# Kernel tuning notes

Measured on AMD Instinct MI355X. Metric: run time of the kernel, lower is better.

Reference implementation:

```python
import jax, jax.numpy as jnp
import numpy as np

B, H, S, D = 2, 16, 2048, 64
NEG_INF = -1e30


def setup_inputs() -> dict:
    key = jax.random.key(0)
    kq, kk, kv = jax.random.split(key, 3)
    one = jnp.ones((1,), dtype=jnp.float32)
    return {
        "q": jax.random.normal(kq, (B, H, S, D), dtype=jnp.float32),
        "k": jax.random.normal(kk, (B, H, S, D), dtype=jnp.float32),
        "v": jax.random.normal(kv, (B, H, S, D), dtype=jnp.float32),
        "d_scale_q": one,
        "d_scale_k": one,
        "d_scale_v": one,
        "q_scale_s": one,
        "q_scale_o": one,
        "d_scale_s": one,
    }


def reference(q, k, v, d_scale_q, d_scale_k, d_scale_v, q_scale_s, q_scale_o, d_scale_s):
    # fp8 fused SDPA math (scales modeled exactly; fp8 rounding omitted in reference)
    scale = 1.0 / jnp.sqrt(jnp.asarray(D, q.dtype))
    qf = q * d_scale_q  # dequantized Q
    kf = k * d_scale_k  # dequantized K
    vf = v * d_scale_v  # dequantized V
    s = jnp.einsum("bhqd,bhkd->bhqk", qf, kf) * scale  # [B,H,S,S]
    # causal mask
    causal = jnp.tril(jnp.ones((S, S), dtype=bool))
    s = jnp.where(causal[None, None], s, NEG_INF)
    p = jax.nn.softmax(s, axis=-1)  # softmax probs
    amax_s = jnp.max(jnp.abs(p))  # amax of softmax output before requant
    # requantize probs (q_scale_s) then dequantize (d_scale_s) for PV matmul
    p_dq = p * (q_scale_s * d_scale_s)
    o_raw = jnp.einsum("bhqk,bhkd->bhqd", p_dq, vf)
    amax_o = jnp.max(jnp.abs(o_raw))  # amax of output before quantization
    o = o_raw * q_scale_o  # quantized-scale output
    return (o, amax_s, amax_o)
```

## Files before the change

### kernel.cpp

```cpp
#include <hip/hip_runtime.h>

#define BB 2
#define HH 16
#define SS 2048
#define DD 64

constexpr int OSIZE = BB * HH * SS * DD;
constexpr float LOG2E = 1.4426950408889634f;

using bf16x8 = __attribute__((ext_vector_type(8))) short;
using f32x4  = __attribute__((ext_vector_type(4))) float;
using u16x8  = __attribute__((ext_vector_type(8))) unsigned short;
using u32x2  = __attribute__((ext_vector_type(2))) unsigned int;
using fl4    = __attribute__((ext_vector_type(4))) float;

__device__ __forceinline__ unsigned short f2bf(float f) {
    unsigned int u = __float_as_uint(f);
    return (unsigned short)((u + 0x7fffu + ((u >> 16) & 1u)) >> 16);
}

__device__ __forceinline__ unsigned int pkbf(float lo, float hi) {
    return __builtin_amdgcn_perm(__float_as_uint(hi), __float_as_uint(lo), 0x07060302u);
}

__device__ __forceinline__ void atomicMaxPosF(float* addr, float v) {
    atomicMax(reinterpret_cast<unsigned int*>(addr), __float_as_uint(v));
}

__global__ __launch_bounds__(256) void prep_kv_kernel(
    const float* __restrict__ k, const float* __restrict__ v,
    const float* __restrict__ dsk, const float* __restrict__ dsv,
    unsigned short* __restrict__ kbf, unsigned short* __restrict__ vtb,
    float* __restrict__ out)
{
    const int t  = threadIdx.x;
    const int s0 = blockIdx.x * 64;
    const int bh = blockIdx.y;
    if (blockIdx.x == 0 && bh == 0 && t < 2) out[OSIZE + t] = 0.0f;

    const size_t base = (size_t)bh * SS * DD;
    const float sck = dsk[0], scv = dsv[0];

    {
        const float* kp = k + base + (size_t)s0 * DD + t * 16;
        unsigned short* ko = kbf + base + (size_t)s0 * DD + t * 16;
        fl4 a0 = ((const fl4*)kp)[0], a1 = ((const fl4*)kp)[1];
        fl4 a2 = ((const fl4*)kp)[2], a3 = ((const fl4*)kp)[3];
        u16x8 o0, o1;
        #pragma unroll
        for (int j = 0; j < 4; ++j) {
            o0[j] = f2bf(a0[j] * sck); o0[j + 4] = f2bf(a1[j] * sck);
            o1[j] = f2bf(a2[j] * sck); o1[j + 4] = f2bf(a3[j] * sck);
        }
        ((u16x8*)ko)[0] = o0; ((u16x8*)ko)[1] = o1;
    }

    __shared__ unsigned short T[64 * 72];
    {
        const int r  = t >> 2;
        const int cb = (t & 3) * 16;
        const fl4* vp = (const fl4*)(v + base + (size_t)(s0 + r) * DD + cb);
        unsigned short tmp[16];
        #pragma unroll
        for (int c = 0; c < 4; ++c) {
            fl4 x = vp[c];
            #pragma unroll
            for (int j = 0; j < 4; ++j) tmp[c * 4 + j] = f2bf(x[j] * scv);
        }
        *(u16x8*)&T[r * 72 + cb]     = *(u16x8*)&tmp[0];
        *(u16x8*)&T[r * 72 + cb + 8] = *(u16x8*)&tmp[8];
    }
    __syncthreads();
    {
        const int dr = t >> 2;
        const int sb = (t & 3) * 16;
        unsigned short tmp[16];
        #pragma unroll
        for (int j = 0; j < 16; ++j) tmp[j] = T[(sb + j) * 72 + dr];
        unsigned short* op = vtb + base + (size_t)dr * SS + s0 + sb;
        *(u16x8*)op       = *(u16x8*)&tmp[0];
        *(u16x8*)(op + 8) = *(u16x8*)&tmp[8];
    }
}

__global__ __launch_bounds__(256, 4) void fattn_kernel(
    const float* __restrict__ q,
    const unsigned short* __restrict__ kbf,
    const unsigned short* __restrict__ vtb,
    const float* __restrict__ dsq, const float* __restrict__ qss,
    const float* __restrict__ qso, const float* __restrict__ dss,
    float* __restrict__ out)
{
    const int x  = blockIdx.x;
    const int bh = blockIdx.y;
    const int tid  = threadIdx.x;
    const int wave = tid >> 6;
    const int lane = tid & 63;
    const int m16  = lane & 15;
    const int quad = lane >> 4;
    const int m7   = m16 & 7;

    __shared__ __align__(16) unsigned short Ksh[2][64 * 64];
    __shared__ __align__(16) unsigned short Vsh[2][64 * 64];
    __shared__ __align__(16) unsigned short Psh[4][16 * 64];

    const float q_scale = dsq[0] * 0.125f * LOG2E;
    const size_t base = (size_t)bh * SS * DD;
    const unsigned short* kbh = kbf + base;
    const unsigned short* vbh = vtb + base;

    const int kr0  = tid >> 3;
    const int kcs  = ((tid & 7) ^ (kr0 & 7)) * 8;
    const int koff0 = kr0 * DD + kcs, koff1 = koff0 + 32 * DD;
    const int voff0 = kr0 * SS + kcs, voff1 = voff0 + 32 * SS;
    const int lds0 = tid * 8, lds1 = (tid + 256) * 8;

    const int gsw0 = (quad ^ m7) * 8;
    const int gsw1 = ((4 | quad) ^ m7) * 8;

    const float ss_ = qss[0] * dss[0];
    const float o_q = qso[0];
    float amax_o = 0.0f, amax_s = 0.0f;

    #pragma unroll
    for (int pass = 0; pass < 2; ++pass) {
        const int qt = pass ? (31 - x) : x;
        const int qb = qt * 64;
        const int nkt = qt + 1;

        bf16x8 qf[2];
        {
            const int qrow = qb + wave * 16 + m16;
            const float* qp = q + base + (size_t)qrow * DD + quad * 8;
            #pragma unroll
            for (int f = 0; f < 2; ++f) {
                fl4 a = *(const fl4*)(qp + f * 32);
                fl4 b = *(const fl4*)(qp + f * 32 + 4);
                #pragma unroll
                for (int j = 0; j < 4; ++j) {
                    qf[f][j]     = (short)f2bf(a[j] * q_scale);
                    qf[f][j + 4] = (short)f2bf(b[j] * q_scale);
                }
            }
        }

        f32x4 Oacc[4];
        #pragma unroll
        for (int dt = 0; dt < 4; ++dt)
            #pragma unroll
            for (int r = 0; r < 4; ++r) Oacc[dt][r] = 0.0f;

        float l_lane = 0.0f, e_max = 0.0f;

        {
            u16x8 k0 = *(const u16x8*)(kbh + koff0);
            u16x8 k1 = *(const u16x8*)(kbh + koff1);
            u16x8 v0 = *(const u16x8*)(vbh + voff0);
            u16x8 v1 = *(const u16x8*)(vbh + voff1);
            *(u16x8*)&Ksh[0][lds0] = k0; *(u16x8*)&Ksh[0][lds1] = k1;
            *(u16x8*)&Vsh[0][lds0] = v0; *(u16x8*)&Vsh[0][lds1] = v1;
        }
        __syncthreads();

        for (int t = 0; t < nkt; ++t) {
            const int b = t & 1;
            const bool pf = (t + 1 < nkt);

            u16x8 kp0, kp1, vp0, vp1;
            if (pf) {
                const unsigned short* kg = kbh + (size_t)(t + 1) * 64 * DD;
                const unsigned short* vg = vbh + (t + 1) * 64;
                kp0 = *(const u16x8*)(kg + koff0);
                kp1 = *(const u16x8*)(kg + koff1);
                vp0 = *(const u16x8*)(vg + voff0);
                vp1 = *(const u16x8*)(vg + voff1);
            }

            const unsigned short* Kt = &Ksh[b][0];
            const unsigned short* Vt = &Vsh[b][0];

            f32x4 sacc[4];
            #pragma unroll
            for (int nt = 0; nt < 4; ++nt) {
                f32x4 acc = {0.0f, 0.0f, 0.0f, 0.0f};
                const int rb = (nt * 16 + m16) * 64;
                bf16x8 kf0 = *(const bf16x8*)&Kt[rb + gsw0];
                bf16x8 kf1 = *(const bf16x8*)&Kt[rb + gsw1];
                acc = __builtin_amdgcn_mfma_f32_16x16x32_bf16(kf0, qf[0], acc, 0, 0, 0);
                acc = __builtin_amdgcn_mfma_f32_16x16x32_bf16(kf1, qf[1], acc, 0, 0, 0);
                sacc[nt] = acc;
            }

            if (t == nkt - 1) {
                const int qg = qb + wave * 16 + m16;
                const int kb = t * 64;
                #pragma unroll
                for (int nt = 0; nt < 4; ++nt)
                    #pragma unroll
                    for (int r = 0; r < 4; ++r) {
                        const int kc = kb + nt * 16 + quad * 4 + r;
                        if (kc > qg) sacc[nt][r] = -1.0e30f;
                    }
            }

            #pragma unroll
            for (int nt = 0; nt < 4; ++nt)
                #pragma unroll
                for (int r = 0; r < 4; ++r) {
                    const float e = __builtin_amdgcn_exp2f(sacc[nt][r]);
                    sacc[nt][r] = e;
                    e_max  = fmaxf(e_max, e);
                    l_lane += e;
                }

            unsigned short* P = &Psh[wave][0];
            #pragma unroll
            for (int nt = 0; nt < 4; ++nt) {
                u32x2 pk;
                pk[0] = pkbf(sacc[nt][0], sacc[nt][1]);
                pk[1] = pkbf(sacc[nt][2], sacc[nt][3]);
                const int g = nt * 2 + (quad >> 1);
                *(u32x2*)&P[m16 * 64 + ((g ^ m7) * 8) + (quad & 1) * 4] = pk;
            }
            bf16x8 pf0 = *(const bf16x8*)&P[m16 * 64 + gsw0];
            bf16x8 pf1 = *(const bf16x8*)&P[m16 * 64 + gsw1];

            #pragma unroll
            for (int dt = 0; dt < 4; ++dt) {
                const int rb = (dt * 16 + m16) * 64;
                bf16x8 vf0 = *(const bf16x8*)&Vt[rb + gsw0];
                bf16x8 vf1 = *(const bf16x8*)&Vt[rb + gsw1];
                Oacc[dt] = __builtin_amdgcn_mfma_f32_16x16x32_bf16(pf0, vf0, Oacc[dt], 0, 0, 0);
                Oacc[dt] = __builtin_amdgcn_mfma_f32_16x16x32_bf16(pf1, vf1, Oacc[dt], 0, 0, 0);
            }

            if (pf) {
                *(u16x8*)&Ksh[b ^ 1][lds0] = kp0; *(u16x8*)&Ksh[b ^ 1][lds1] = kp1;
                *(u16x8*)&Vsh[b ^ 1][lds0] = vp0; *(u16x8*)&Vsh[b ^ 1][lds1] = vp1;
            }
            __syncthreads();
        }

        float l = l_lane;
        l += __shfl_xor(l, 16);
        l += __shfl_xor(l, 32);
        float em = e_max;
        em = fmaxf(em, __shfl_xor(em, 16));
        em = fmaxf(em, __shfl_xor(em, 32));
        amax_s = fmaxf(amax_s, em / l);

        #pragma unroll
        for (int r = 0; r < 4; ++r) {
            const float lr  = __shfl(l, (lane & 48) | (quad * 4 + r));
            const float ivl = ss_ / lr;
            const int row = qb + wave * 16 + quad * 4 + r;
            float* op = out + base + (size_t)row * DD + m16;
            #pragma unroll
            for (int dt = 0; dt < 4; ++dt) {
                const float o_raw = Oacc[dt][r] * ivl;
                amax_o = fmaxf(amax_o, fabsf(o_raw));
                op[dt * 16] = o_raw * o_q;
            }
        }
    }

    #pragma unroll
    for (int m = 1; m < 64; m <<= 1) {
        amax_o = fmaxf(amax_o, __shfl_xor(amax_o, m));
        amax_s = fmaxf(amax_s, __shfl_xor(amax_s, m));
    }
    if (lane == 0) {
        atomicMaxPosF(out + OSIZE,     amax_s);
        atomicMaxPosF(out + OSIZE + 1, amax_o);
    }
}

extern "C" void kernel_launch(void* const* d_in, const int* in_sizes, int n_in,
                              void* d_out, int out_size, void* d_ws, size_t ws_size,
                              hipStream_t stream) {
    const float* q   = (const float*)d_in[0];
    const float* k   = (const float*)d_in[1];
    const float* v   = (const float*)d_in[2];
    const float* dsq = (const float*)d_in[3];
    const float* dsk = (const float*)d_in[4];
    const float* dsv = (const float*)d_in[5];
    const float* qss = (const float*)d_in[6];
    const float* qso = (const float*)d_in[7];
    const float* dss = (const float*)d_in[8];
    float* out = (float*)d_out;

    unsigned short* kbf = (unsigned short*)d_ws;
    unsigned short* vtb = (unsigned short*)d_ws + OSIZE;

    prep_kv_kernel<<<dim3(SS / 64, BB * HH), 256, 0, stream>>>(k, v, dsk, dsv, kbf, vtb, out);

    dim3 grid(16, BB * HH);
    fattn_kernel<<<grid, 256, 0, stream>>>(q, kbf, vtb, dsq, qss, qso, dss, out);
}
```

Measured before the change: 184.5 us.

## Split KV tiles across two wave groups per block and combine partials in LDS

Blocks grow to 512 threads, split into two groups of four waves. Each group processes alternating KV tiles for the same query tile with its own double-buffered K/V LDS, then group 1 hands its O accumulator and row sums to group 0 through LDS for the final normalisation. This is meant to halve each block's serial KV loop and raise the number of waves per CU. The cost is double the LDS per block, an extra combine step with barriers, and odd tile counts that leave one group idle on the last iteration. The grid is also reordered so that bh is the fast-varying block index.

```diff
diff --git a/kernel.cpp b/kernel.cpp
--- a/kernel.cpp
+++ b/kernel.cpp
@@ -83,7 +83,7 @@
     }
 }
 
-__global__ __launch_bounds__(256, 4) void fattn_kernel(
+__global__ __launch_bounds__(512, 4) void fattn_kernel(
     const float* __restrict__ q,
     const unsigned short* __restrict__ kbf,
     const unsigned short* __restrict__ vtb,
@@ -91,29 +91,32 @@
     const float* __restrict__ qso, const float* __restrict__ dss,
     float* __restrict__ out)
 {
-    const int x  = blockIdx.x;
-    const int bh = blockIdx.y;
-    const int tid  = threadIdx.x;
-    const int wave = tid >> 6;
-    const int lane = tid & 63;
-    const int m16  = lane & 15;
-    const int quad = lane >> 4;
-    const int m7   = m16 & 7;
-
-    __shared__ __align__(16) unsigned short Ksh[2][64 * 64];
-    __shared__ __align__(16) unsigned short Vsh[2][64 * 64];
-    __shared__ __align__(16) unsigned short Psh[4][16 * 64];
+    const int bh = blockIdx.x;
+    const int x  = blockIdx.y;
+    const int tid   = threadIdx.x;
+    const int group = tid >> 8;
+    const int tg    = tid & 255;
+    const int wave  = tid >> 6;
+    const int gw    = wave & 3;
+    const int lane  = tid & 63;
+    const int m16   = lane & 15;
+    const int quad  = lane >> 4;
+    const int m7    = m16 & 7;
+
+    __shared__ __align__(16) unsigned short Ksh[2][2][64 * 64];
+    __shared__ __align__(16) unsigned short Vsh[2][2][64 * 64];
+    __shared__ __align__(16) unsigned short Psh[8][16 * 64];
 
     const float q_scale = dsq[0] * 0.125f * LOG2E;
     const size_t base = (size_t)bh * SS * DD;
     const unsigned short* kbh = kbf + base;
     const unsigned short* vbh = vtb + base;
 
-    const int kr0  = tid >> 3;
-    const int kcs  = ((tid & 7) ^ (kr0 & 7)) * 8;
+    const int kr0  = tg >> 3;
+    const int kcs  = ((tg & 7) ^ (kr0 & 7)) * 8;
     const int koff0 = kr0 * DD + kcs, koff1 = koff0 + 32 * DD;
     const int voff0 = kr0 * SS + kcs, voff1 = voff0 + 32 * SS;
-    const int lds0 = tid * 8, lds1 = (tid + 256) * 8;
+    const int lds0 = tg * 8, lds1 = (tg + 256) * 8;
 
     const int gsw0 = (quad ^ m7) * 8;
     const int gsw1 = ((4 | quad) ^ m7) * 8;
@@ -122,15 +125,18 @@
     const float o_q = qso[0];
     float amax_o = 0.0f, amax_s = 0.0f;
 
-    #pragma unroll
+    float* CombO = (float*)&Ksh[1][0][0];
+    float* CombL = (float*)&Vsh[1][0][0];
+
     for (int pass = 0; pass < 2; ++pass) {
         const int qt = pass ? (31 - x) : x;
         const int qb = qt * 64;
         const int nkt = qt + 1;
+        const int n_iter = (nkt + 1) >> 1;
 
         bf16x8 qf[2];
         {
-            const int qrow = qb + wave * 16 + m16;
+            const int qrow = qb + gw * 16 + m16;
             const float* qp = q + base + (size_t)qrow * DD + quad * 8;
             #pragma unroll
             for (int f = 0; f < 2; ++f) {
@@ -149,129 +155,157 @@
         for (int dt = 0; dt < 4; ++dt)
             #pragma unroll
             for (int r = 0; r < 4; ++r) Oacc[dt][r] = 0.0f;
-
         float l_lane = 0.0f, e_max = 0.0f;
 
-        {
-            u16x8 k0 = *(const u16x8*)(kbh + koff0);
-            u16x8 k1 = *(const u16x8*)(kbh + koff1);
-            u16x8 v0 = *(const u16x8*)(vbh + voff0);
-            u16x8 v1 = *(const u16x8*)(vbh + voff1);
-            *(u16x8*)&Ksh[0][lds0] = k0; *(u16x8*)&Ksh[0][lds1] = k1;
-            *(u16x8*)&Vsh[0][lds0] = v0; *(u16x8*)&Vsh[0][lds1] = v1;
+        if (group < nkt) {
+            const unsigned short* kg = kbh + (size_t)group * 64 * DD;
+            const unsigned short* vg = vbh + group * 64;
+            u16x8 k0 = *(const u16x8*)(kg + koff0);
+            u16x8 k1 = *(const u16x8*)(kg + koff1);
+            u16x8 v0 = *(const u16x8*)(vg + voff0);
+            u16x8 v1 = *(const u16x8*)(vg + voff1);
+            *(u16x8*)&Ksh[group][0][lds0] = k0; *(u16x8*)&Ksh[group][0][lds1] = k1;
+            *(u16x8*)&Vsh[group][0][lds0] = v0; *(u16x8*)&Vsh[group][0][lds1] = v1;
         }
         __syncthreads();
 
-        for (int t = 0; t < nkt; ++t) {
-            const int b = t & 1;
-            const bool pf = (t + 1 < nkt);
+        for (int j = 0; j < n_iter; ++j) {
+            const int b  = j & 1;
+            const int tt = 2 * j + group;
+            const int tn = tt + 2;
+            const bool pfv = (tn < nkt);
 
             u16x8 kp0, kp1, vp0, vp1;
-            if (pf) {
-                const unsigned short* kg = kbh + (size_t)(t + 1) * 64 * DD;
-                const unsigned short* vg = vbh + (t + 1) * 64;
+            if (pfv) {
+                const unsigned short* kg = kbh + (size_t)tn * 64 * DD;
+                const unsigned short* vg = vbh + tn * 64;
                 kp0 = *(const u16x8*)(kg + koff0);
                 kp1 = *(const u16x8*)(kg + koff1);
                 vp0 = *(const u16x8*)(vg + voff0);
                 vp1 = *(const u16x8*)(vg + voff1);
             }
 
-            const unsigned short* Kt = &Ksh[b][0];
-            const unsigned short* Vt = &Vsh[b][0];
-
-            f32x4 sacc[4];
-            #pragma unroll
-            for (int nt = 0; nt < 4; ++nt) {
-                f32x4 acc = {0.0f, 0.0f, 0.0f, 0.0f};
-                const int rb = (nt * 16 + m16) * 64;
-                bf16x8 kf0 = *(const bf16x8*)&Kt[rb + gsw0];
-                bf16x8 kf1 = *(const bf16x8*)&Kt[rb + gsw1];
-                acc = __builtin_amdgcn_mfma_f32_16x16x32_bf16(kf0, qf[0], acc, 0, 0, 0);
-                acc = __builtin_amdgcn_mfma_f32_16x16x32_bf16(kf1, qf[1], acc, 0, 0, 0);
-                sacc[nt] = acc;
-            }
-
-            if (t == nkt - 1) {
-                const int qg = qb + wave * 16 + m16;
-                const int kb = t * 64;
+            if (tt < nkt) {
+                const unsigned short* Kt = &Ksh[group][b][0];
+                const unsigned short* Vt = &Vsh[group][b][0];
+
+                f32x4 sacc[4];
+                #pragma unroll
+                for (int nt = 0; nt < 4; ++nt) {
+                    f32x4 acc = {0.0f, 0.0f, 0.0f, 0.0f};
+                    const int rb = (nt * 16 + m16) * 64;
+                    bf16x8 kf0 = *(const bf16x8*)&Kt[rb + gsw0];
+                    bf16x8 kf1 = *(const bf16x8*)&Kt[rb + gsw1];
+                    acc = __builtin_amdgcn_mfma_f32_16x16x32_bf16(kf0, qf[0], acc, 0, 0, 0);
+                    acc = __builtin_amdgcn_mfma_f32_16x16x32_bf16(kf1, qf[1], acc, 0, 0, 0);
+                    sacc[nt] = acc;
+                }
+
+                if (tt == nkt - 1) {
+                    const int qg = qb + gw * 16 + m16;
+                    const int kb = tt * 64;
+                    #pragma unroll
+                    for (int nt = 0; nt < 4; ++nt)
+                        #pragma unroll
+                        for (int r = 0; r < 4; ++r) {
+                            const int kc = kb + nt * 16 + quad * 4 + r;
+                            if (kc > qg) sacc[nt][r] = -1.0e30f;
+                        }
+                }
+
                 #pragma unroll
                 for (int nt = 0; nt < 4; ++nt)
                     #pragma unroll
                     for (int r = 0; r < 4; ++r) {
-                        const int kc = kb + nt * 16 + quad * 4 + r;
-                        if (kc > qg) sacc[nt][r] = -1.0e30f;
+                        const float e = __builtin_amdgcn_exp2f(sacc[nt][r]);
+                        sacc[nt][r] = e;
+                        e_max  = fmaxf(e_max, e);
+                        l_lane += e;
                     }
-            }
-
-            #pragma unroll
-            for (int nt = 0; nt < 4; ++nt)
-                #pragma unroll
-                for (int r = 0; r < 4; ++r) {
-                    const float e = __builtin_amdgcn_exp2f(sacc[nt][r]);
-                    sacc[nt][r] = e;
-                    e_max  = fmaxf(e_max, e);
-                    l_lane += e;
-                }
-
-            unsigned short* P = &Psh[wave][0];
-            #pragma unroll
-            for (int nt = 0; nt < 4; ++nt) {
-                u32x2 pk;
-                pk[0] = pkbf(sacc[nt][0], sacc[nt][1]);
-                pk[1] = pkbf(sacc[nt][2], sacc[nt][3]);
-                const int g = nt * 2 + (quad >> 1);
-                *(u32x2*)&P[m16 * 64 + ((g ^ m7) * 8) + (quad & 1) * 4] = pk;
-            }
-            bf16x8 pf0 = *(const bf16x8*)&P[m16 * 64 + gsw0];
-            bf16x8 pf1 = *(const bf16x8*)&P[m16 * 64 + gsw1];
-
+
+                unsigned short* P = &Psh[wave][0];
+                #pragma unroll
+                for (int nt = 0; nt < 4; ++nt) {
+                    u32x2 pk;
+                    pk[0] = pkbf(sacc[nt][0], sacc[nt][1]);
+                    pk[1] = pkbf(sacc[nt][2], sacc[nt][3]);
+                    const int g = nt * 2 + (quad >> 1);
+                    *(u32x2*)&P[m16 * 64 + ((g ^ m7) * 8) + (quad & 1) * 4] = pk;
+                }
+                bf16x8 pf0 = *(const bf16x8*)&P[m16 * 64 + gsw0];
+                bf16x8 pf1 = *(const bf16x8*)&P[m16 * 64 + gsw1];
+
+                #pragma unroll
+                for (int dt = 0; dt < 4; ++dt) {
+                    const int rb = (dt * 16 + m16) * 64;
+                    bf16x8 vf0 = *(const bf16x8*)&Vt[rb + gsw0];
+                    bf16x8 vf1 = *(const bf16x8*)&Vt[rb + gsw1];
+                    Oacc[dt] = __builtin_amdgcn_mfma_f32_16x16x32_bf16(pf0, vf0, Oacc[dt], 0, 0, 0);
+                    Oacc[dt] = __builtin_amdgcn_mfma_f32_16x16x32_bf16(pf1, vf1, Oacc[dt], 0, 0, 0);
+                }
+            }
+
+            if (pfv) {
+                *(u16x8*)&Ksh[group][b ^ 1][lds0] = kp0; *(u16x8*)&Ksh[group][b ^ 1][lds1] = kp1;
+                *(u16x8*)&Vsh[group][b ^ 1][lds0] = vp0; *(u16x8*)&Vsh[group][b ^ 1][lds1] = vp1;
+            }
+            __syncthreads();
+        }
+
+        if (group == 1) {
+            float* co = CombO + gw * 1024;
+            #pragma unroll
+            for (int dt = 0; dt < 4; ++dt) *(f32x4*)(co + dt * 256 + lane * 4) = Oacc[dt];
+            CombL[gw * 64 + lane]       = l_lane;
+            CombL[256 + gw * 64 + lane] = e_max;
+        }
+        __syncthreads();
+        if (group == 0) {
+            const float* co = CombO + gw * 1024;
             #pragma unroll
             for (int dt = 0; dt < 4; ++dt) {
-                const int rb = (dt * 16 + m16) * 64;
-                bf16x8 vf0 = *(const bf16x8*)&Vt[rb + gsw0];
-                bf16x8 vf1 = *(const bf16x8*)&Vt[rb + gsw1];
-                Oacc[dt] = __builtin_amdgcn_mfma_f32_16x16x32_bf16(pf0, vf0, Oacc[dt], 0, 0, 0);
-                Oacc[dt] = __builtin_amdgcn_mfma_f32_16x16x32_bf16(pf1, vf1, Oacc[dt], 0, 0, 0);
-            }
-
-            if (pf) {
-                *(u16x8*)&Ksh[b ^ 1][lds0] = kp0; *(u16x8*)&Ksh[b ^ 1][lds1] = kp1;
-                *(u16x8*)&Vsh[b ^ 1][lds0] = vp0; *(u16x8*)&Vsh[b ^ 1][lds1] = vp1;
-            }
-            __syncthreads();
-        }
-
-        float l = l_lane;
-        l += __shfl_xor(l, 16);
-        l += __shfl_xor(l, 32);
-        float em = e_max;
-        em = fmaxf(em, __shfl_xor(em, 16));
-        em = fmaxf(em, __shfl_xor(em, 32));
-        amax_s = fmaxf(amax_s, em / l);
-
-        #pragma unroll
-        for (int r = 0; r < 4; ++r) {
-            const float lr  = __shfl(l, (lane & 48) | (quad * 4 + r));
-            const float ivl = ss_ / lr;
-            const int row = qb + wave * 16 + quad * 4 + r;
-            float* op = out + base + (size_t)row * DD + m16;
-            #pragma unroll
-            for (int dt = 0; dt < 4; ++dt) {
-                const float o_raw = Oacc[dt][r] * ivl;
-                amax_o = fmaxf(amax_o, fabsf(o_raw));
-                op[dt * 16] = o_raw * o_q;
-            }
-        }
-    }
-
-    #pragma unroll
-    for (int m = 1; m < 64; m <<= 1) {
-        amax_o = fmaxf(amax_o, __shfl_xor(amax_o, m));
-        amax_s = fmaxf(amax_s, __shfl_xor(amax_s, m));
-    }
-    if (lane == 0) {
-        atomicMaxPosF(out + OSIZE,     amax_s);
-        atomicMaxPosF(out + OSIZE + 1, amax_o);
+                f32x4 add = *(const f32x4*)(co + dt * 256 + lane * 4);
+                #pragma unroll
+                for (int r = 0; r < 4; ++r) Oacc[dt][r] += add[r];
+            }
+            l_lane += CombL[gw * 64 + lane];
+            e_max   = fmaxf(e_max, CombL[256 + gw * 64 + lane]);
+
+            float l = l_lane;
+            l += __shfl_xor(l, 16);
+            l += __shfl_xor(l, 32);
+            float em = e_max;
+            em = fmaxf(em, __shfl_xor(em, 16));
+            em = fmaxf(em, __shfl_xor(em, 32));
+            amax_s = fmaxf(amax_s, em / l);
+
+            #pragma unroll
+            for (int r = 0; r < 4; ++r) {
+                const float lr  = __shfl(l, (lane & 48) | (quad * 4 + r));
+                const float ivl = ss_ / lr;
+                const int row = qb + gw * 16 + quad * 4 + r;
+                float* op = out + base + (size_t)row * DD + m16;
+                #pragma unroll
+                for (int dt = 0; dt < 4; ++dt) {
+                    const float o_raw = Oacc[dt][r] * ivl;
+                    amax_o = fmaxf(amax_o, fabsf(o_raw));
+                    op[dt * 16] = o_raw * o_q;
+                }
+            }
+        }
+        __syncthreads();
+    }
+
+    if (group == 0) {
+        #pragma unroll
+        for (int m = 1; m < 64; m <<= 1) {
+            amax_o = fmaxf(amax_o, __shfl_xor(amax_o, m));
+            amax_s = fmaxf(amax_s, __shfl_xor(amax_s, m));
+        }
+        if (lane == 0) {
+            atomicMaxPosF(out + OSIZE,     amax_s);
+            atomicMaxPosF(out + OSIZE + 1, amax_o);
+        }
     }
 }
 
@@ -294,6 +328,6 @@
 
     prep_kv_kernel<<<dim3(SS / 64, BB * HH), 256, 0, stream>>>(k, v, dsk, dsv, kbf, vtb, out);
 
-    dim3 grid(16, BB * HH);
-    fattn_kernel<<<grid, 256, 0, stream>>>(q, kbf, vtb, dsq, qss, qso, dss, out);
-}
+    dim3 grid(BB * HH, 16);
+    fattn_kernel<<<grid, 512, 0, stream>>>(q, kbf, vtb, dsq, qss, qso, dss, out);
+}
```

After: 178.0 us. 1.04x faster.
